# Performance work log

Hardware: AMD Instinct MI355X
Metric: run time of the kernel (lower is better)

Reference implementation:

```python
import jax, jax.numpy as jnp
import numpy as np

NUM_STEPS = 20
BETA = 0.9
THR = 1.0
B, D, H, O = 8192, 784, 128, 10


def setup_inputs() -> dict:
    key = jax.random.key(0)
    k1, k2, k3, k4, k5 = jax.random.split(key, 5)
    x = jax.random.uniform(k1, (B, D), jnp.float32)  # rates in [0,1]
    lim1 = 1.0 / np.sqrt(D)
    lim2 = 1.0 / np.sqrt(H)
    fc1_w = jax.random.uniform(k2, (H, D), jnp.float32, -lim1, lim1)
    fc1_b = jax.random.uniform(k3, (H,), jnp.float32, -lim1, lim1)
    fc2_w = jax.random.uniform(k4, (O, H), jnp.float32, -lim2, lim2)
    fc2_b = jax.random.uniform(k5, (O,), jnp.float32, -lim2, lim2)
    return {"x": x, "fc1_w": fc1_w, "fc1_b": fc1_b, "fc2_w": fc2_w, "fc2_b": fc2_b}


def heaviside(u):
    return (u > 0).astype(u.dtype)


def lif_step(mem, cur):
    # snntorch Leaky, reset_mechanism='subtract':
    #   reset computed from incoming mem, then mem = beta*mem + cur - reset*thr
    reset = heaviside(mem - THR)
    mem = BETA * mem + cur - reset * THR
    spk = heaviside(mem - THR)
    return spk, mem


def reference(x, fc1_w, fc1_b, fc2_w, fc2_b):
    batch = x.shape[0]
    # spikegen.rate: per-step Bernoulli with probability x (fixed key -> deterministic)
    skey = jax.random.key(42)
    x_spike = jax.random.bernoulli(skey, x, (NUM_STEPS, batch, x.shape[1])).astype(x.dtype)

    mem1 = jnp.zeros((batch, fc1_w.shape[0]), x.dtype)
    mem2 = jnp.zeros((batch, fc2_w.shape[0]), x.dtype)

    def step(carry, x_t):
        m1, m2 = carry
        cur1 = x_t @ fc1_w.T + fc1_b          # [B,128]
        spk1, m1 = lif_step(m1, cur1)
        cur2 = spk1 @ fc2_w.T + fc2_b         # [B,10]
        spk2, m2 = lif_step(m2, cur2)
        return (m1, m2), spk2

    _, spk2_stack = jax.lax.scan(step, (mem1, mem2), x_spike)  # [T,B,10]
    return spk2_stack.sum(axis=0) / NUM_STEPS
```

## Files before the change

kernel.cpp:

```cpp
#include <hip/hip_runtime.h>
#include <cstdint>


#define T_STEPS 20
#define B_SZ   8192
#define D_SZ   784
#define H_SZ   128
#define O_SZ   10
#define CUR1_BYTES  83886080u
#define MASKS_OFF   83886080u
#define WP_OFF      84541440u
#define M32_OFF     85155840u
#define THR_OFF     101539840u

typedef __attribute__((ext_vector_type(8))) short short8;
typedef __attribute__((ext_vector_type(4))) float f32x4;
typedef unsigned short ushort_t;

#define ROTL_ASM(dst, src, sh)                                        \
  asm("v_alignbit_b32 %0, %1, %1, %2" : "=v"(dst) : "v"(src), "n"(32 - (sh)))

__device__ __forceinline__ void threefry_0_42(uint32_t c0, uint32_t c1,
                                              uint32_t& o0, uint32_t& o1) {
  const uint32_t ks0 = 0u;
  const uint32_t ks1 = 42u;
  const uint32_t ks2 = 0u ^ 42u ^ 0x1BD11BDAu;
  uint32_t x0 = c0 + ks0;
  uint32_t x1 = c1 + ks1;
  uint32_t r;
#define TF_R(rot) { x0 += x1; ROTL_ASM(r, x1, rot); x1 = r ^ x0; }
  TF_R(13) TF_R(15) TF_R(26) TF_R(6)
  x0 += ks1; x1 += ks2 + 1u;
  TF_R(17) TF_R(29) TF_R(16) TF_R(24)
  x0 += ks2; x1 += ks0 + 2u;
  TF_R(13) TF_R(15) TF_R(26) TF_R(6)
  x0 += ks0; x1 += ks1 + 3u;
  TF_R(17) TF_R(29) TF_R(16) TF_R(24)
  x0 += ks1; x1 += ks2 + 4u;
  TF_R(13) TF_R(15) TF_R(26) TF_R(6)
  x0 += ks2; x1 += ks0 + 5u;
#undef TF_R
  o0 = x0; o1 = x1;
}

__device__ __forceinline__ uint32_t rne_bf16_bits(float f) {
  uint32_t u = __float_as_uint(f);
  return (u + 0x7fffu + ((u >> 16) & 1u)) & 0xffff0000u;
}

__global__ __launch_bounds__(256) void prep(
    const float* __restrict__ w1, const float* __restrict__ x,
    ushort_t* __restrict__ wp, uint32_t* __restrict__ thresh) {
  if (blockIdx.x < 128) {
    const int h = blockIdx.x;
    for (int k = threadIdx.x; k < 800; k += 256) {
      float w = (k < D_SZ) ? w1[h * D_SZ + k] : 0.0f;
      uint32_t hb = rne_bf16_bits(w);
      float hi = __uint_as_float(hb);
      float r1 = w - hi;
      uint32_t mb = rne_bf16_bits(r1);
      float mid = __uint_as_float(mb);
      float lo = r1 - mid;
      uint32_t lb = __float_as_uint(lo);
      wp[0 * 102400 + h * 800 + k] = (ushort_t)(hb >> 16);
      wp[1 * 102400 + h * 800 + k] = (ushort_t)(mb >> 16);
      wp[2 * 102400 + h * 800 + k] = (ushort_t)(lb >> 16);
    }
  } else {
    const int gid = (blockIdx.x - 128) * 256 + threadIdx.x;
    const int b = gid / 100;
    const int y = gid - b * 100;
    const int d0 = y << 3;
    uint4 T0 = {0u, 0u, 0u, 0u}, T1 = {0u, 0u, 0u, 0u};
    if (y < 98) {
      const float* xr = x + (size_t)b * D_SZ + d0;
      float4 v0 = *(const float4*)xr;
      float4 v1 = *(const float4*)(xr + 4);
      T0.x = (uint32_t)__builtin_ceilf(v0.x * 8388608.0f);
      T0.y = (uint32_t)__builtin_ceilf(v0.y * 8388608.0f);
      T0.z = (uint32_t)__builtin_ceilf(v0.z * 8388608.0f);
      T0.w = (uint32_t)__builtin_ceilf(v0.w * 8388608.0f);
      T1.x = (uint32_t)__builtin_ceilf(v1.x * 8388608.0f);
      T1.y = (uint32_t)__builtin_ceilf(v1.y * 8388608.0f);
      T1.z = (uint32_t)__builtin_ceilf(v1.z * 8388608.0f);
      T1.w = (uint32_t)__builtin_ceilf(v1.w * 8388608.0f);
    }
    uint32_t* tp = thresh + (size_t)b * 800 + d0;
    *(uint4*)tp       = T0;
    *(uint4*)(tp + 4) = T1;
  }
}

__global__ __launch_bounds__(256) void spikegen_bits(
    const uint32_t* __restrict__ thresh, uint8_t* __restrict__ m8) {
  const int g  = blockIdx.x * 256 + threadIdx.x;
  const int tb = g / 100;
  const int y  = g - tb * 100;
  const int b  = tb & 8191;
  const int d0 = y << 3;

  const uint32_t* tp = thresh + (size_t)b * 800 + d0;
  uint4 T0 = *(const uint4*)tp;
  uint4 T1 = *(const uint4*)(tp + 4);
  uint32_t T[8] = {T0.x, T0.y, T0.z, T0.w, T1.x, T1.y, T1.z, T1.w};

  const uint32_t nb = (uint32_t)tb * 784u + (uint32_t)d0;
  uint32_t mybyte = 0u;
#pragma unroll
  for (int j = 0; j < 8; ++j) {
    uint32_t o0, o1;
    threefry_0_42(0u, nb + (uint32_t)j, o0, o1);
    mybyte |= (((o0 ^ o1) >> 9) < T[j]) ? (1u << j) : 0u;
  }
  m8[g] = (uint8_t)mybyte;
}

__global__ __launch_bounds__(256) void gemm1_mfma(
    const ushort_t* __restrict__ wp, const uint32_t* __restrict__ m32,
    const float* __restrict__ b1, float* __restrict__ cur1) {
  const int tid  = threadIdx.x;
  const int row0 = blockIdx.x << 7;
  const int wave = tid >> 6, lane = tid & 63;
  const int wr0  = (wave >> 1) << 6;
  const int wc0  = (wave & 1) << 6;
  const int lm   = lane & 15, quad = lane >> 4;
  const int qsh  = quad << 3;

  f32x4 acc[4][4];
#pragma unroll
  for (int m = 0; m < 4; ++m)
#pragma unroll
    for (int nn = 0; nn < 4; ++nn) acc[m][nn] = (f32x4){0.f, 0.f, 0.f, 0.f};

  const uint32_t* mrow = m32 + (size_t)(row0 + wr0 + lm) * 25;
  const ushort_t* wbase = wp + (size_t)(wc0 + lm) * 800 + qsh;

  for (int ko = 0; ko < 25; ++ko) {
    short8 a[4];
#pragma unroll
    for (int m = 0; m < 4; ++m) {
      uint32_t word = mrow[m * 400 + ko];
      uint32_t byte = (word >> qsh) & 0xffu;
      short8 av;
#pragma unroll
      for (int j = 0; j < 8; ++j)
        av[j] = (short)(((byte >> j) & 1u) ? 0x3F80 : 0);
      a[m] = av;
    }
    const int kof = ko << 5;
#pragma unroll
    for (int p = 0; p < 3; ++p) {
#pragma unroll
      for (int nn = 0; nn < 4; ++nn) {
        short8 bf = *(const short8*)&wbase[p * 102400 + nn * 16 * 800 + kof];
#pragma unroll
        for (int m = 0; m < 4; ++m)
          acc[m][nn] = __builtin_amdgcn_mfma_f32_16x16x32_bf16(
              a[m], bf, acc[m][nn], 0, 0, 0);
      }
    }
  }

#pragma unroll
  for (int nn = 0; nn < 4; ++nn) {
    int col = wc0 + nn * 16 + lm;
    float bias = b1[col];
#pragma unroll
    for (int m = 0; m < 4; ++m) {
#pragma unroll
      for (int r = 0; r < 4; ++r) {
        int grow = row0 + wr0 + m * 16 + quad * 4 + r;
        cur1[(size_t)grow * H_SZ + col] = acc[m][nn][r] + bias;
      }
    }
  }
}

__global__ __launch_bounds__(256) void lif1_spikes(
    const float* __restrict__ cur1, uint32_t* __restrict__ masks) {
#pragma clang fp contract(off)
  const int g    = blockIdx.x * 256 + threadIdx.x;
  const int row  = g >> 4;
  const int s    = g & 15;
  const int lane = threadIdx.x & 63;

  float mem[8];
#pragma unroll
  for (int i = 0; i < 8; ++i) mem[i] = 0.0f;

  for (int t = 0; t < T_STEPS; ++t) {
    const float* base = cur1 + ((size_t)t * B_SZ + row) * H_SZ + s * 8;
    float4 c0 = *(const float4*)base;
    float4 c1 = *(const float4*)(base + 4);
    float cv[8] = {c0.x, c0.y, c0.z, c0.w, c1.x, c1.y, c1.z, c1.w};

    uint32_t bits8 = 0u;
#pragma unroll
    for (int q = 0; q < 8; ++q) {
      float m = mem[q];
      float reset = (m > 1.0f) ? 1.0f : 0.0f;
      m = 0.9f * m;
      m = m + cv[q];
      m = m - reset;
      mem[q] = m;
      bits8 |= (m > 1.0f) ? (1u << q) : 0u;
    }
    uint32_t part = bits8 << ((s & 3) * 8);
    part |= __shfl_xor(part, 1);
    part |= __shfl_xor(part, 2);
    uint32_t myw = __shfl(part, (lane & ~15) + 4 * (s & 3));
    if (s < 4)
      masks[((size_t)t * B_SZ + row) * 4 + s] = myw;
  }
}

__global__ __launch_bounds__(320) void lif2_seq(
    const float* __restrict__ w2, const float* __restrict__ b2,
    const uint32_t* __restrict__ masks, float* __restrict__ out) {
#pragma clang fp contract(off)
  __shared__ __align__(16) float sW2[O_SZ][H_SZ];
  const int tid = threadIdx.x;
  for (int i = tid; i < O_SZ * H_SZ; i += 320)
    sW2[i >> 7][i & 127] = w2[i];
  __syncthreads();

  const int wave = tid >> 6;
  const int lane = tid & 63;
  const int row  = ((blockIdx.x >> 1) << 6) + lane;
  const int o    = (blockIdx.x & 1) * 5 + wave;
  const float bias = b2[o];

  float mem2 = 0.0f;
  int cnt = 0;
  const uint4* mbase = (const uint4*)masks;

  for (int t = 0; t < T_STEPS; ++t) {
    uint4 m = mbase[(size_t)t * B_SZ + row];
    uint32_t mw[4] = {m.x, m.y, m.z, m.w};
    float acc = 0.0f;
#pragma unroll
    for (int w = 0; w < 4; ++w) {
#pragma unroll
      for (int hc = 0; hc < 8; ++hc) {
        float4 wv = *(const float4*)&sW2[o][w * 32 + hc * 4];
        float vv[4] = {wv.x, wv.y, wv.z, wv.w};
#pragma unroll
        for (int bb = 0; bb < 4; ++bb) {
          float val = ((mw[w] >> (hc * 4 + bb)) & 1u) ? vv[bb] : 0.0f;
          acc = acc + val;
        }
      }
    }
    float c2 = acc + bias;
    float reset = (mem2 > 1.0f) ? 1.0f : 0.0f;
    mem2 = 0.9f * mem2;
    mem2 = mem2 + c2;
    mem2 = mem2 - reset;
    cnt += (mem2 > 1.0f) ? 1 : 0;
  }
  out[row * O_SZ + o] = (float)cnt / 20.0f;
}

extern "C" void kernel_launch(void* const* d_in, const int* in_sizes, int n_in,
                              void* d_out, int out_size, void* d_ws, size_t ws_size,
                              hipStream_t stream) {
  const float* x   = (const float*)d_in[0];
  const float* w1  = (const float*)d_in[1];
  const float* b1  = (const float*)d_in[2];
  const float* w2  = (const float*)d_in[3];
  const float* b2  = (const float*)d_in[4];
  float* out  = (float*)d_out;
  float*    cur1   = (float*)d_ws;
  uint32_t* masks  = (uint32_t*)((char*)d_ws + MASKS_OFF);
  ushort_t* wp     = (ushort_t*)((char*)d_ws + WP_OFF);
  uint32_t* m32    = (uint32_t*)((char*)d_ws + M32_OFF);
  uint8_t*  m8     = (uint8_t*)((char*)d_ws + M32_OFF);
  uint32_t* thresh = (uint32_t*)((char*)d_ws + THR_OFF);

  prep         <<<dim3(3328),  dim3(256), 0, stream>>>(w1, x, wp, thresh);
  spikegen_bits<<<dim3(64000), dim3(256), 0, stream>>>(thresh, m8);
  gemm1_mfma   <<<dim3(1280),  dim3(256), 0, stream>>>(wp, m32, b1, cur1);
  lif1_spikes  <<<dim3(512),   dim3(256), 0, stream>>>(cur1, masks);
  lif2_seq     <<<dim3(256),   dim3(320), 0, stream>>>(w2, b2, masks, out);
}
```

Before: 453.1 us.

## Fuse Bernoulli spike generation into GEMM1 via shared-memory bitmasks

Removes the separate spikegen_bits kernel and generates the threefry-based spike bitmask inside the GEMM kernel, storing 128x25 packed words per block in LDS instead of writing and re-reading a global mask buffer. Thresholds are pre-shifted by 9 so the comparison can use the raw random bits, and the bit packing uses a compare plus add-with-carry asm sequence. This drops one kernel launch and the global round trip of the mask array. In exchange, the RNG work now runs serially before the MFMA loop in each block, which may underuse the GEMM's parallelism and add LDS pressure. Each thread also holds 32 thresholds in registers, which raises register use.

```diff
diff --git a/kernel.cpp b/kernel.cpp
--- a/kernel.cpp
+++ b/kernel.cpp
@@ -10,7 +10,6 @@
 #define CUR1_BYTES  83886080u
 #define MASKS_OFF   83886080u
 #define WP_OFF      84541440u
-#define M32_OFF     85155840u
 #define THR_OFF     101539840u
 
 typedef __attribute__((ext_vector_type(8))) short short8;
@@ -76,14 +75,14 @@
       const float* xr = x + (size_t)b * D_SZ + d0;
       float4 v0 = *(const float4*)xr;
       float4 v1 = *(const float4*)(xr + 4);
-      T0.x = (uint32_t)__builtin_ceilf(v0.x * 8388608.0f);
-      T0.y = (uint32_t)__builtin_ceilf(v0.y * 8388608.0f);
-      T0.z = (uint32_t)__builtin_ceilf(v0.z * 8388608.0f);
-      T0.w = (uint32_t)__builtin_ceilf(v0.w * 8388608.0f);
-      T1.x = (uint32_t)__builtin_ceilf(v1.x * 8388608.0f);
-      T1.y = (uint32_t)__builtin_ceilf(v1.y * 8388608.0f);
-      T1.z = (uint32_t)__builtin_ceilf(v1.z * 8388608.0f);
-      T1.w = (uint32_t)__builtin_ceilf(v1.w * 8388608.0f);
+      T0.x = (uint32_t)__builtin_ceilf(v0.x * 8388608.0f) << 9;
+      T0.y = (uint32_t)__builtin_ceilf(v0.y * 8388608.0f) << 9;
+      T0.z = (uint32_t)__builtin_ceilf(v0.z * 8388608.0f) << 9;
+      T0.w = (uint32_t)__builtin_ceilf(v0.w * 8388608.0f) << 9;
+      T1.x = (uint32_t)__builtin_ceilf(v1.x * 8388608.0f) << 9;
+      T1.y = (uint32_t)__builtin_ceilf(v1.y * 8388608.0f) << 9;
+      T1.z = (uint32_t)__builtin_ceilf(v1.z * 8388608.0f) << 9;
+      T1.w = (uint32_t)__builtin_ceilf(v1.w * 8388608.0f) << 9;
     }
     uint32_t* tp = thresh + (size_t)b * 800 + d0;
     *(uint4*)tp       = T0;
@@ -91,35 +90,42 @@
   }
 }
 
-__global__ __launch_bounds__(256) void spikegen_bits(
-    const uint32_t* __restrict__ thresh, uint8_t* __restrict__ m8) {
-  const int g  = blockIdx.x * 256 + threadIdx.x;
-  const int tb = g / 100;
-  const int y  = g - tb * 100;
-  const int b  = tb & 8191;
-  const int d0 = y << 3;
-
-  const uint32_t* tp = thresh + (size_t)b * 800 + d0;
-  uint4 T0 = *(const uint4*)tp;
-  uint4 T1 = *(const uint4*)(tp + 4);
-  uint32_t T[8] = {T0.x, T0.y, T0.z, T0.w, T1.x, T1.y, T1.z, T1.w};
-
-  const uint32_t nb = (uint32_t)tb * 784u + (uint32_t)d0;
-  uint32_t mybyte = 0u;
-#pragma unroll
-  for (int j = 0; j < 8; ++j) {
-    uint32_t o0, o1;
-    threefry_0_42(0u, nb + (uint32_t)j, o0, o1);
-    mybyte |= (((o0 ^ o1) >> 9) < T[j]) ? (1u << j) : 0u;
-  }
-  m8[g] = (uint8_t)mybyte;
-}
-
-__global__ __launch_bounds__(256) void gemm1_mfma(
-    const ushort_t* __restrict__ wp, const uint32_t* __restrict__ m32,
+__global__ __launch_bounds__(256) void spike_gemm(
+    const uint32_t* __restrict__ thresh, const ushort_t* __restrict__ wp,
     const float* __restrict__ b1, float* __restrict__ cur1) {
+  __shared__ uint32_t sM[128 * 25];
+
   const int tid  = threadIdx.x;
   const int row0 = blockIdx.x << 7;
+  const int b0   = (blockIdx.x & 63) << 7;
+
+  for (int idx = tid; idx < 3200; idx += 256) {
+    int r = idx / 25;
+    int w = idx - r * 25;
+    int b = b0 + r;
+    const uint32_t* tp = thresh + (size_t)b * 800 + (w << 5);
+    uint32_t Ts[32];
+#pragma unroll
+    for (int q = 0; q < 8; ++q) {
+      uint4 v = *(const uint4*)(tp + q * 4);
+      Ts[q * 4 + 0] = v.x; Ts[q * 4 + 1] = v.y;
+      Ts[q * 4 + 2] = v.z; Ts[q * 4 + 3] = v.w;
+    }
+    const uint32_t nw = (uint32_t)(row0 + r) * 784u + ((uint32_t)w << 5);
+    uint32_t word = 0u;
+#pragma unroll
+    for (int j = 31; j >= 0; --j) {
+      uint32_t o0, o1;
+      threefry_0_42(0u, nw + (uint32_t)j, o0, o1);
+      uint32_t bits = o0 ^ o1;
+      asm("v_cmp_lt_u32 vcc, %1, %2\n\t"
+          "v_addc_co_u32 %0, vcc, %0, %0, vcc"
+          : "+v"(word) : "v"(bits), "v"(Ts[j]) : "vcc");
+    }
+    sM[idx] = word;
+  }
+  __syncthreads();
+
   const int wave = tid >> 6, lane = tid & 63;
   const int wr0  = (wave >> 1) << 6;
   const int wc0  = (wave & 1) << 6;
@@ -132,8 +138,8 @@
 #pragma unroll
     for (int nn = 0; nn < 4; ++nn) acc[m][nn] = (f32x4){0.f, 0.f, 0.f, 0.f};
 
-  const uint32_t* mrow = m32 + (size_t)(row0 + wr0 + lm) * 25;
   const ushort_t* wbase = wp + (size_t)(wc0 + lm) * 800 + qsh;
+  const uint32_t* mrow  = &sM[(wr0 + lm) * 25];
 
   for (int ko = 0; ko < 25; ++ko) {
     short8 a[4];
@@ -273,13 +279,10 @@
   float*    cur1   = (float*)d_ws;
   uint32_t* masks  = (uint32_t*)((char*)d_ws + MASKS_OFF);
   ushort_t* wp     = (ushort_t*)((char*)d_ws + WP_OFF);
-  uint32_t* m32    = (uint32_t*)((char*)d_ws + M32_OFF);
-  uint8_t*  m8     = (uint8_t*)((char*)d_ws + M32_OFF);
   uint32_t* thresh = (uint32_t*)((char*)d_ws + THR_OFF);
 
-  prep         <<<dim3(3328),  dim3(256), 0, stream>>>(w1, x, wp, thresh);
-  spikegen_bits<<<dim3(64000), dim3(256), 0, stream>>>(thresh, m8);
-  gemm1_mfma   <<<dim3(1280),  dim3(256), 0, stream>>>(wp, m32, b1, cur1);
-  lif1_spikes  <<<dim3(512),   dim3(256), 0, stream>>>(cur1, masks);
-  lif2_seq     <<<dim3(256),   dim3(320), 0, stream>>>(w2, b2, masks, out);
-}
+  prep       <<<dim3(3328), dim3(256), 0, stream>>>(w1, x, wp, thresh);
+  spike_gemm <<<dim3(1280), dim3(256), 0, stream>>>(thresh, wp, b1, cur1);
+  lif1_spikes<<<dim3(512),  dim3(256), 0, stream>>>(cur1, masks);
+  lif2_seq   <<<dim3(256),  dim3(320), 0, stream>>>(w2, b2, masks, out);
+}
```

Measured after the change: 444.4 us. About the same (-1.9%).
